# Kernel optimization log

Hardware: AMD Instinct MI355X
Metric: run time of the kernel (lower is better)

The kernel has to match this reference:

```python
import jax, jax.numpy as jnp
import numpy as np

STRIDE = 8
MIN_CONFIDENCE = 0.1


def setup_inputs() -> dict:
    key = jax.random.key(0)
    k1, k2, k3 = jax.random.split(key, 3)
    B, h, w = 4, 68, 120
    Hf, Wf = h * STRIDE, w * STRIDE
    # per-cell gaussian centers in full-res pixel coords, (x, y) ordering
    mean = jax.random.uniform(k1, (B, h, w, 2), dtype=jnp.float32) * jnp.array([Wf, Hf], jnp.float32)
    # variance in px^2 (sigma roughly 2..8 px)
    variance = jax.random.uniform(k2, (B, h, w), dtype=jnp.float32) * 60.0 + 4.0
    confidence = jax.random.uniform(k3, (B, h, w), dtype=jnp.float32)
    return {"mean": mean, "variance": variance, "confidence": confidence}


def reference(mean, variance, confidence):
    # Faithful to DecodePIFLayer.__dynamic_loop_over_cells_with_max_implementation:
    # acc[b,y,x] = sum over cells j with conf[b,j] > MIN_CONFIDENCE of
    #   exp(-((x - mx)^2 + (y - my)^2) / (2*var)) * conf
    # Expressed as separable-Gaussian outer products + a batched GEMM
    # (mathematically identical; thresholded cells contribute exactly 0).
    B, h, w, _ = mean.shape
    Hf, Wf = h * STRIDE, w * STRIDE
    X = jnp.arange(Wf, dtype=mean.dtype)  # positions[..., 0]
    Y = jnp.arange(Hf, dtype=mean.dtype)  # positions[..., 1]

    mx = mean[..., 0].reshape(B, -1)            # [B, J]
    my = mean[..., 1].reshape(B, -1)            # [B, J]
    inv2v = 1.0 / (2.0 * variance.reshape(B, -1))  # [B, J]
    conf = confidence.reshape(B, -1)
    conf_m = jnp.where(conf > MIN_CONFIDENCE, conf, 0.0)  # [B, J]

    # gy: [B, J, Hf], gx: [B, J, Wf] (confidence folded into gx)
    gy = jnp.exp(-((Y[None, None, :] - my[:, :, None]) ** 2) * inv2v[:, :, None])
    gx = jnp.exp(-((X[None, None, :] - mx[:, :, None]) ** 2) * inv2v[:, :, None]) * conf_m[:, :, None]
    acc = jnp.einsum('bjy,bjx->byx', gy, gx)  # [B, Hf, Wf]
    return acc
```

## Files before the change

kernel.cpp:

```cpp
#include <hip/hip_runtime.h>

#define B_ 4
#define J_ 8160
#define HF 544
#define WF 960
#define TS 32
#define TXN 30
#define TYN 17
#define NPX 15
#define NPPB (NPX*TYN)
#define R2COEF 23.0259f

typedef _Float16 half8 __attribute__((ext_vector_type(8)));
typedef float floatx16 __attribute__((ext_vector_type(16)));

__global__ __launch_bounds__(256, 4) void pif_pair(const float2* __restrict__ mean,
                                                   const float*  __restrict__ var,
                                                   const float*  __restrict__ conf,
                                                   float* __restrict__ out) {
    __shared__ float4 qbuf[4][256];
    int wid  = threadIdx.x >> 6;
    int lane = threadIdx.x & 63;
    int pair = blockIdx.x;
    int b    = blockIdx.y;

    int pty = pair / NPX;
    int ptx = pair - pty * NPX;

    const float4* mb4 = (const float4*)(mean + (size_t)b * J_);
    const float2* vb2 = (const float2*)(var  + (size_t)b * J_);
    const float2* cb2 = (const float2*)(conf + (size_t)b * J_);

    float4* q = qbuf[wid];
    int qn = 0;

    float x0 = (float)(ptx * 64), y0 = (float)(pty * TS);
    float x1 = x0 + 63.f,         y1 = y0 + 31.f;
    int   lx = lane & 31, half = lane >> 5;
    float xfL = x0 + (float)lx;
    float xfR = x0 + 32.f + (float)lx;
    float yf  = y0 + (float)lx;
    const unsigned long long below = (1ull << lane) - 1ull;

    floatx16 accL = {}, accR = {};

    auto drain16 = [&](int base) {
        half8 af, bfl, bfr;
        #pragma unroll
        for (int i = 0; i < 8; ++i) {
            float4 e = q[base + 8 * half + i];
            float dy  = yf  - e.y;
            float dxl = xfL - e.x;
            float dxr = xfR - e.x;
            af[i]  = (_Float16)__expf(-dy * dy * e.z);
            float c = e.w;
            bfl[i] = (_Float16)(c * __expf(-dxl * dxl * e.z));
            bfr[i] = (_Float16)(c * __expf(-dxr * dxr * e.z));
        }
        accL = __builtin_amdgcn_mfma_f32_32x32x16_f16(af, bfl, accL, 0, 0, 0);
        accR = __builtin_amdgcn_mfma_f32_32x32x16_f16(af, bfr, accR, 0, 0, 0);
    };

    int jbase = wid * 2048;
    for (int s = 0; s < 16; ++s) {
        int j0 = jbase + s * 128 + 2 * lane;
        bool valid = j0 < J_;
        int  jh = (valid ? j0 : 0) >> 1;

        float4 mm = mb4[jh];
        float2 vv = vb2[jh];
        float2 cc = cb2[jh];

        float cx0 = fminf(fmaxf(mm.x, x0), x1);
        float cy0 = fminf(fmaxf(mm.y, y0), y1);
        float cx1 = fminf(fmaxf(mm.z, x0), x1);
        float cy1 = fminf(fmaxf(mm.w, y0), y1);
        float dx0 = mm.x - cx0, dy0 = mm.y - cy0;
        float dx1 = mm.z - cx1, dy1 = mm.w - cy1;
        bool p0 = valid & (cc.x > 0.1f) & (dx0 * dx0 + dy0 * dy0 <= R2COEF * vv.x);
        bool p1 = valid & (cc.y > 0.1f) & (dx1 * dx1 + dy1 * dy1 <= R2COEF * vv.y);

        unsigned long long m0 = __ballot(p0);
        if (p0) q[qn + __popcll(m0 & below)] =
            make_float4(mm.x, mm.y, __builtin_amdgcn_rcpf(2.0f * vv.x), cc.x);
        qn += __popcll(m0);
        if (__builtin_expect(qn >= 144, 0)) {
            while (qn >= 16) { qn -= 16; drain16(qn); }
        }
        unsigned long long m1 = __ballot(p1);
        if (p1) q[qn + __popcll(m1 & below)] =
            make_float4(mm.z, mm.w, __builtin_amdgcn_rcpf(2.0f * vv.y), cc.y);
        qn += __popcll(m1);
        if (__builtin_expect(qn >= 144, 0)) {
            while (qn >= 16) { qn -= 16; drain16(qn); }
        }
    }

    while (qn >= 16) { qn -= 16; drain16(qn); }
    if (qn > 0) {
        if (lane >= qn && lane < 16)
            q[lane] = make_float4(0.f, 0.f, 0.f, 0.f);
        drain16(0);
    }

    float (*red)[32][32] = (float (*)[32][32])qbuf;
    int th = threadIdx.x;

    __syncthreads();
    #pragma unroll
    for (int r = 0; r < 16; ++r) {
        int row = (r & 3) + 8 * (r >> 2) + 4 * half;
        red[wid][row][lx] = accL[r];
    }
    __syncthreads();
    #pragma unroll
    for (int k = 0; k < 4; ++k) {
        int p   = th + 256 * k;
        int row = p >> 5, col = p & 31;
        float s = red[0][row][col] + red[1][row][col]
                + red[2][row][col] + red[3][row][col];
        out[((size_t)(b * HF + pty * TS + row)) * WF + (ptx * 64 + col)] = s;
    }

    __syncthreads();
    #pragma unroll
    for (int r = 0; r < 16; ++r) {
        int row = (r & 3) + 8 * (r >> 2) + 4 * half;
        red[wid][row][lx] = accR[r];
    }
    __syncthreads();
    #pragma unroll
    for (int k = 0; k < 4; ++k) {
        int p   = th + 256 * k;
        int row = p >> 5, col = p & 31;
        float s = red[0][row][col] + red[1][row][col]
                + red[2][row][col] + red[3][row][col];
        out[((size_t)(b * HF + pty * TS + row)) * WF + (ptx * 64 + 32 + col)] = s;
    }
}

extern "C" void kernel_launch(void* const* d_in, const int* in_sizes, int n_in,
                              void* d_out, int out_size, void* d_ws, size_t ws_size,
                              hipStream_t stream) {
    const float2* mean = (const float2*)d_in[0];
    const float*  var  = (const float*)d_in[1];
    const float*  conf = (const float*)d_in[2];
    float* out = (float*)d_out;
    (void)d_ws; (void)ws_size;

    pif_pair<<<dim3(NPPB, B_), 256, 0, stream>>>(mean, var, conf, out);
}
```

Before: 19.36 us.

## Widen per-block tile to three 32-column MFMA tiles sharing one cell scan

Each block now covers a 32x96 output region using three MFMA accumulators instead of two, so the per-block scan, culling and queueing of all cells, plus the y-gaussian evaluation, are shared across more output. The grid shrinks accordingly. The trade-off is a wider culling box that admits more cells per block, higher register pressure, and fewer blocks for load balancing.

Result: no change. 19.40 us (+0.2%).

```diff
diff --git a/kernel.cpp b/kernel.cpp
--- a/kernel.cpp
+++ b/kernel.cpp
@@ -5,27 +5,26 @@
 #define HF 544
 #define WF 960
 #define TS 32
-#define TXN 30
 #define TYN 17
-#define NPX 15
-#define NPPB (NPX*TYN)
+#define NTX 10
+#define NTPB (NTX*TYN)
 #define R2COEF 23.0259f
 
 typedef _Float16 half8 __attribute__((ext_vector_type(8)));
 typedef float floatx16 __attribute__((ext_vector_type(16)));
 
-__global__ __launch_bounds__(256, 4) void pif_pair(const float2* __restrict__ mean,
-                                                   const float*  __restrict__ var,
-                                                   const float*  __restrict__ conf,
-                                                   float* __restrict__ out) {
+__global__ __launch_bounds__(256, 4) void pif_tri(const float2* __restrict__ mean,
+                                                  const float*  __restrict__ var,
+                                                  const float*  __restrict__ conf,
+                                                  float* __restrict__ out) {
     __shared__ float4 qbuf[4][256];
     int wid  = threadIdx.x >> 6;
     int lane = threadIdx.x & 63;
-    int pair = blockIdx.x;
+    int tri  = blockIdx.x;
     int b    = blockIdx.y;
 
-    int pty = pair / NPX;
-    int ptx = pair - pty * NPX;
+    int pty = tri / NTX;
+    int ptx = tri - pty * NTX;
 
     const float4* mb4 = (const float4*)(mean + (size_t)b * J_);
     const float2* vb2 = (const float2*)(var  + (size_t)b * J_);
@@ -34,30 +33,34 @@
     float4* q = qbuf[wid];
     int qn = 0;
 
-    float x0 = (float)(ptx * 64), y0 = (float)(pty * TS);
-    float x1 = x0 + 63.f,         y1 = y0 + 31.f;
+    float x0 = (float)(ptx * 96), y0 = (float)(pty * TS);
+    float x1 = x0 + 95.f,         y1 = y0 + 31.f;
     int   lx = lane & 31, half = lane >> 5;
     float xfL = x0 + (float)lx;
-    float xfR = x0 + 32.f + (float)lx;
+    float xfM = x0 + 32.f + (float)lx;
+    float xfR = x0 + 64.f + (float)lx;
     float yf  = y0 + (float)lx;
     const unsigned long long below = (1ull << lane) - 1ull;
 
-    floatx16 accL = {}, accR = {};
+    floatx16 accL = {}, accM = {}, accR = {};
 
     auto drain16 = [&](int base) {
-        half8 af, bfl, bfr;
+        half8 af, bfl, bfm, bfr;
         #pragma unroll
         for (int i = 0; i < 8; ++i) {
             float4 e = q[base + 8 * half + i];
             float dy  = yf  - e.y;
             float dxl = xfL - e.x;
+            float dxm = xfM - e.x;
             float dxr = xfR - e.x;
             af[i]  = (_Float16)__expf(-dy * dy * e.z);
             float c = e.w;
             bfl[i] = (_Float16)(c * __expf(-dxl * dxl * e.z));
+            bfm[i] = (_Float16)(c * __expf(-dxm * dxm * e.z));
             bfr[i] = (_Float16)(c * __expf(-dxr * dxr * e.z));
         }
         accL = __builtin_amdgcn_mfma_f32_32x32x16_f16(af, bfl, accL, 0, 0, 0);
+        accM = __builtin_amdgcn_mfma_f32_32x32x16_f16(af, bfm, accM, 0, 0, 0);
         accR = __builtin_amdgcn_mfma_f32_32x32x16_f16(af, bfr, accR, 0, 0, 0);
     };
 
@@ -106,36 +109,25 @@
     float (*red)[32][32] = (float (*)[32][32])qbuf;
     int th = threadIdx.x;
 
-    __syncthreads();
     #pragma unroll
-    for (int r = 0; r < 16; ++r) {
-        int row = (r & 3) + 8 * (r >> 2) + 4 * half;
-        red[wid][row][lx] = accL[r];
-    }
-    __syncthreads();
-    #pragma unroll
-    for (int k = 0; k < 4; ++k) {
-        int p   = th + 256 * k;
-        int row = p >> 5, col = p & 31;
-        float s = red[0][row][col] + red[1][row][col]
-                + red[2][row][col] + red[3][row][col];
-        out[((size_t)(b * HF + pty * TS + row)) * WF + (ptx * 64 + col)] = s;
-    }
-
-    __syncthreads();
-    #pragma unroll
-    for (int r = 0; r < 16; ++r) {
-        int row = (r & 3) + 8 * (r >> 2) + 4 * half;
-        red[wid][row][lx] = accR[r];
-    }
-    __syncthreads();
-    #pragma unroll
-    for (int k = 0; k < 4; ++k) {
-        int p   = th + 256 * k;
-        int row = p >> 5, col = p & 31;
-        float s = red[0][row][col] + red[1][row][col]
-                + red[2][row][col] + red[3][row][col];
-        out[((size_t)(b * HF + pty * TS + row)) * WF + (ptx * 64 + 32 + col)] = s;
+    for (int pass = 0; pass < 3; ++pass) {
+        const floatx16& a = (pass == 0) ? accL : (pass == 1) ? accM : accR;
+        __syncthreads();
+        #pragma unroll
+        for (int r = 0; r < 16; ++r) {
+            int row = (r & 3) + 8 * (r >> 2) + 4 * half;
+            red[wid][row][lx] = a[r];
+        }
+        __syncthreads();
+        #pragma unroll
+        for (int k = 0; k < 4; ++k) {
+            int p   = th + 256 * k;
+            int row = p >> 5, col = p & 31;
+            float s = red[0][row][col] + red[1][row][col]
+                    + red[2][row][col] + red[3][row][col];
+            out[((size_t)(b * HF + pty * TS + row)) * WF
+                + (ptx * 96 + pass * 32 + col)] = s;
+        }
     }
 }
 
@@ -148,5 +140,5 @@
     float* out = (float*)d_out;
     (void)d_ws; (void)ws_size;
 
-    pif_pair<<<dim3(NPPB, B_), 256, 0, stream>>>(mean, var, conf, out);
+    pif_tri<<<dim3(NTPB, B_), 256, 0, stream>>>(mean, var, conf, out);
 }
```
